# Kernel optimization log

Hardware: AMD Instinct MI355X
Metric: run time of the kernel (lower is better)

Reference implementation:

```python
import jax, jax.numpy as jnp
import numpy as np

V, E, H, L = 10000, 512, 512, 3   # vocab, embed dim, hidden, num decoder layers
SOS, EOS = 1, 2


def setup_inputs() -> dict:
    key = jax.random.key(0)
    ks = jax.random.split(key, 16)
    N, To, Ti = 32, 64, 512
    s = 0.05
    inp = {
        'padded_input': jax.random.randint(ks[0], (N, To), 0, V),
        'encoder_padded_outputs': jax.random.normal(ks[1], (N, Ti, H), jnp.float32),
        'emb': jax.random.normal(ks[2], (V, E), jnp.float32) * s,
        # layer 0 LSTMCell: input = embed + encoder context (E + H)
        'W_ih0': jax.random.normal(ks[3], (4 * H, E + H), jnp.float32) * s,
        'W_hh0': jax.random.normal(ks[4], (4 * H, H), jnp.float32) * s,
        'b_ih0': jnp.zeros((4 * H,), jnp.float32),
        'b_hh0': jnp.zeros((4 * H,), jnp.float32),
        # layers 1..L-1 LSTMCells (stacked)
        'W_ih_r': jax.random.normal(ks[5], (L - 1, 4 * H, H), jnp.float32) * s,
        'W_hh_r': jax.random.normal(ks[6], (L - 1, 4 * H, H), jnp.float32) * s,
        'b_ih_r': jnp.zeros((L - 1, 4 * H), jnp.float32),
        'b_hh_r': jnp.zeros((L - 1, 4 * H), jnp.float32),
        # MLP: Linear(2H -> H), Tanh, Linear(H -> V)
        'W1': jax.random.normal(ks[7], (H, 2 * H), jnp.float32) * s,
        'b1': jnp.zeros((H,), jnp.float32),
        'W2': jax.random.normal(ks[8], (V, H), jnp.float32) * s,
        'b2': jnp.zeros((V,), jnp.float32),
    }
    return inp


def _lstm_cell(x, h, c, Wi, Wh, bi, bh):
    # torch.nn.LSTMCell gate order: i, f, g, o
    g = x @ Wi.T + h @ Wh.T + bi + bh
    i, f, gg, o = jnp.split(g, 4, axis=-1)
    c2 = jax.nn.sigmoid(f) * c + jax.nn.sigmoid(i) * jnp.tanh(gg)
    h2 = jax.nn.sigmoid(o) * jnp.tanh(c2)
    return h2, c2


def reference(padded_input, encoder_padded_outputs, emb,
              W_ih0, W_hh0, b_ih0, b_hh0,
              W_ih_r, W_hh_r, b_ih_r, b_hh_r,
              W1, b1, W2, b2):
    N, To = padded_input.shape
    sos = jnp.full((N, 1), SOS, padded_input.dtype)
    eos = jnp.full((N, 1), EOS, padded_input.dtype)
    ys_in = jnp.concatenate([sos, padded_input], axis=1)    # [N, T]
    ys_out = jnp.concatenate([padded_input, eos], axis=1)   # [N, T]
    xs = jnp.transpose(emb[ys_in], (1, 0, 2))               # [T, N, E]

    def step(carry, x_t):
        h, c, att_c = carry                                  # h,c: [L,N,H]; att_c: [N,H]
        rnn_in = jnp.concatenate([x_t, att_c], axis=1)       # [N, E+H]
        h0, c0 = _lstm_cell(rnn_in, h[0], c[0], W_ih0, W_hh0, b_ih0, b_hh0)
        hs, cs = [h0], [c0]
        for l in range(L - 1):
            hl, cl = _lstm_cell(hs[-1], h[l + 1], c[l + 1],
                                W_ih_r[l], W_hh_r[l], b_ih_r[l], b_hh_r[l])
            hs.append(hl); cs.append(cl)
        r = hs[-1]                                           # [N, H]
        scores = jnp.einsum('nh,nth->nt', r, encoder_padded_outputs)
        w = jax.nn.softmax(scores, axis=-1)
        att = jnp.einsum('nt,nth->nh', w, encoder_padded_outputs)
        mlp_in = jnp.concatenate([r, att], axis=1)           # [N, 2H]
        y = jnp.tanh(mlp_in @ W1.T + b1) @ W2.T + b2         # [N, V]
        return (jnp.stack(hs), jnp.stack(cs), att), y

    h0 = jnp.zeros((L, N, H), encoder_padded_outputs.dtype)
    c0 = jnp.zeros((L, N, H), encoder_padded_outputs.dtype)
    a0 = jnp.zeros((N, H), encoder_padded_outputs.dtype)
    _, ys = jax.lax.scan(step, (h0, c0, a0), xs)             # [T, N, V]
    y_all = jnp.transpose(ys, (1, 0, 2))                     # [N, T, V]

    logp = jax.nn.log_softmax(y_all, axis=-1)
    nll = -jnp.take_along_axis(logp, ys_out[..., None], axis=-1)[..., 0]
    ce_loss = nll.mean()
    return y_all, ce_loss
```

## Files before the change

kernel.cpp:

```cpp
#include <hip/hip_runtime.h>
#include <hip/hip_bf16.h>
#include <hip/hip_fp16.h>

#define NB 32
#define TO 64
#define TT 65
#define TI 512
#define VV 10000
#define HH 512
#define G4 2048
#define SOS_ID 1
#define EOS_ID 2
#define NBLK 256

typedef unsigned uvec4 __attribute__((ext_vector_type(4)));
typedef unsigned uvec2 __attribute__((ext_vector_type(2)));
typedef _Float16 h2v __attribute__((ext_vector_type(2)));

__device__ __forceinline__ float cload1(const float* p) {
    unsigned v = __hip_atomic_load((const unsigned*)p,
                                   __ATOMIC_RELAXED, __HIP_MEMORY_SCOPE_AGENT);
    return __uint_as_float(v);
}
__device__ __forceinline__ float2 cload2(const float* p) {
    unsigned long long v = __hip_atomic_load((const unsigned long long*)p,
                                             __ATOMIC_RELAXED, __HIP_MEMORY_SCOPE_AGENT);
    float2 r;
    r.x = __uint_as_float((unsigned)(v & 0xffffffffull));
    r.y = __uint_as_float((unsigned)(v >> 32));
    return r;
}
__device__ __forceinline__ void cstore(float* p, float v) {
    __hip_atomic_store((unsigned*)p, __float_as_uint(v),
                       __ATOMIC_RELAXED, __HIP_MEMORY_SCOPE_AGENT);
}

__device__ __forceinline__ void gbar(int* flags, int g, int s, int& epoch) {
    asm volatile("s_waitcnt vmcnt(0) lgkmcnt(0)" ::: "memory");
    __syncthreads();
    epoch++;
    int tid = threadIdx.x;
    if (tid == 0)
        __hip_atomic_store(&flags[(g * 32 + s) * 16], epoch,
                           __ATOMIC_RELAXED, __HIP_MEMORY_SCOPE_AGENT);
    if (tid < 32) {
        for (;;) {
            int v = __hip_atomic_load(&flags[(g * 32 + tid) * 16],
                                      __ATOMIC_RELAXED, __HIP_MEMORY_SCOPE_AGENT);
            unsigned long long b = __ballot(v >= epoch);
            if ((b & 0xffffffffull) == 0xffffffffull) break;
            __builtin_amdgcn_s_sleep(1);
        }
    }
    __syncthreads();
}

__device__ __forceinline__ float bf2f(unsigned u16) {
    return __uint_as_float(u16 << 16);
}
__device__ __forceinline__ unsigned f2bf(float f) {
    unsigned u = __float_as_uint(f);
    return (u + 0x7fffu + ((u >> 16) & 1u)) >> 16;
}
__device__ __forceinline__ unsigned packh2(float a, float b) {
    __half2 h = __floats2half2_rn(a, b);
    return *(unsigned*)&h;
}
__device__ __forceinline__ h2v uash2(unsigned u) {
    union { unsigned u; h2v h; } c; c.u = u; return c.h;
}

template <int KQ4>
__device__ __forceinline__ void lstm_phase(
    const unsigned* __restrict__ Wtb, const float* __restrict__ bi,
    const float* __restrict__ bh, float* __restrict__ hout,
    float& creg, float* __restrict__ mlprow,
    float4* xs4, float* sg, float* sg2, int s, int n0,
    const float* __restrict__ pre) {
    int tid = threadIdx.x;
    int lane = tid & 63, wv = tid >> 6;
    const uvec2* wp = (const uvec2*)Wtb + (long)(wv * KQ4) * 2048 + (s * 64 + lane);
    const float4* xp = (const float4*)xs4 + wv * KQ4 * 4;
    float a0 = 0.f, a1 = 0.f, a2 = 0.f, a3 = 0.f;
#pragma unroll 4
    for (int kq = 0; kq < KQ4; kq++) {
        uvec2 u = wp[(long)kq * 2048];
        float w0 = bf2f(u.x & 0xffffu), w1 = bf2f(u.x >> 16);
        float w2 = bf2f(u.y & 0xffffu), w3 = bf2f(u.y >> 16);
        float4 x0 = xp[4 * kq], x1 = xp[4 * kq + 1];
        float4 x2 = xp[4 * kq + 2], x3 = xp[4 * kq + 3];
        a0 = fmaf(w0, x0.x, a0); a1 = fmaf(w0, x0.y, a1);
        a2 = fmaf(w0, x0.z, a2); a3 = fmaf(w0, x0.w, a3);
        a0 = fmaf(w1, x1.x, a0); a1 = fmaf(w1, x1.y, a1);
        a2 = fmaf(w1, x1.z, a2); a3 = fmaf(w1, x1.w, a3);
        a0 = fmaf(w2, x2.x, a0); a1 = fmaf(w2, x2.y, a1);
        a2 = fmaf(w2, x2.z, a2); a3 = fmaf(w2, x2.w, a3);
        a0 = fmaf(w3, x3.x, a0); a1 = fmaf(w3, x3.y, a1);
        a2 = fmaf(w3, x3.z, a2); a3 = fmaf(w3, x3.w, a3);
    }
    float4 r4; r4.x = a0; r4.y = a1; r4.z = a2; r4.w = a3;
    ((float4*)sg)[wv * 64 + lane] = r4;
    __syncthreads();
    {
        int c = tid >> 4, n = (tid >> 2) & 3, w4 = tid & 3;
        float sum = sg[((w4 * 4 + 0) * 64 + c) * 4 + n]
                  + sg[((w4 * 4 + 1) * 64 + c) * 4 + n]
                  + sg[((w4 * 4 + 2) * 64 + c) * 4 + n]
                  + sg[((w4 * 4 + 3) * 64 + c) * 4 + n];
        sg2[tid] = sum;
    }
    __syncthreads();
    if (tid < 64) {
        int gn = tid >> 4, gml = tid & 15, gm = s * 16 + gml;
        float ga[4];
#pragma unroll
        for (int q = 0; q < 4; q++) {
            int c = q * 16 + gml;
            const float* p = sg2 + c * 16 + gn * 4;
            ga[q] = p[0] + p[1] + p[2] + p[3];
        }
        float gi = ga[0] + bi[gm] + bh[gm];
        float gf = ga[1] + bi[512 + gm] + bh[512 + gm];
        float gg = ga[2] + bi[1024 + gm] + bh[1024 + gm];
        float go = ga[3] + bi[1536 + gm] + bh[1536 + gm];
        float si = 1.f / (1.f + expf(-gi));
        float sf = 1.f / (1.f + expf(-gf));
        float so = 1.f / (1.f + expf(-go));
        float c2 = sf * creg + si * tanhf(gg);
        creg = c2;
        float hv = so * tanhf(c2);
        cstore(&hout[(n0 + gn) * 512 + gm], hv);
        if (mlprow) mlprow[(long)(n0 + gn) * 1024 + gm] = hv;
    } else if (pre && tid >= 512 && tid < 768) {
        int k = 512 + (tid - 512) * 2;
        float2 va = cload2(pre + (n0 + 0) * 512 + (k - 512));
        float2 vb = cload2(pre + (n0 + 1) * 512 + (k - 512));
        float2 vc = cload2(pre + (n0 + 2) * 512 + (k - 512));
        float2 vd = cload2(pre + (n0 + 3) * 512 + (k - 512));
        float4 x0, x1;
        x0.x = va.x; x0.y = vb.x; x0.z = vc.x; x0.w = vd.x;
        x1.x = va.y; x1.y = vb.y; x1.z = vc.y; x1.w = vd.y;
        xs4[k] = x0; xs4[k + 1] = x1;
    }
}

__global__ __launch_bounds__(1024, 4) void decode_loop(
    const unsigned* __restrict__ Wtb0, const unsigned* __restrict__ Wtb1,
    const unsigned* __restrict__ Wtb2, const float* __restrict__ emb,
    const int* __restrict__ tokens, const float* __restrict__ enc,
    const float* __restrict__ b_ih0, const float* __restrict__ b_hh0,
    const float* __restrict__ b_ih_r, const float* __restrict__ b_hh_r,
    float* __restrict__ hbuf, float* __restrict__ pvec, float* __restrict__ pm,
    float* __restrict__ mlpin, int* flags) {
    __shared__ float4 xs4[1536];
    __shared__ float sg[4096];
    __shared__ float sg2[1024];
    __shared__ float wl[64];
    __shared__ unsigned short enct[32768];

    int tid = threadIdx.x, b = blockIdx.x;
    int g = b >> 5, s = b & 31;
    int epoch = 0;
    int n0 = g * 4;
    int na = n0 + (s >> 3), tiq = s & 7;
    float c0r = 0.f, c1r = 0.f, c2r = 0.f;

    {
        int tl = tid >> 4;
        int gb = (tid & 15) * 4;
        const float* ebase = enc + ((long)na * TI + tiq * 64 + tl) * HH;
#pragma unroll
        for (int q = 0; q < 4; q++) {
            int gg = gb + q;
            const float* ep = ebase + gg * 8;
            float4 lo = *(const float4*)ep;
            float4 hi = *(const float4*)(ep + 4);
            uvec4 pk;
            pk.x = f2bf(lo.x) | (f2bf(lo.y) << 16);
            pk.y = f2bf(lo.z) | (f2bf(lo.w) << 16);
            pk.z = f2bf(hi.x) | (f2bf(hi.y) << 16);
            pk.w = f2bf(hi.z) | (f2bf(hi.w) << 16);
            *(uvec4*)(enct + tl * 512 + (gg ^ (tl & 7)) * 8) = pk;
        }
    }
    __syncthreads();

    for (int t = 0; t < TT; t++) {
        int rp = t & 1;
        float* hOld = hbuf + rp * 3 * NB * HH;
        float* hNew = hbuf + (rp ^ 1) * 3 * NB * HH;
        float* h0r = hOld;
        float* h1r = hOld + NB * HH;
        float* h2r = hOld + 2 * NB * HH;
        float* h0w = hNew;
        float* h1w = hNew + NB * HH;
        float* h2w = hNew + 2 * NB * HH;

        if (t == 0) {
            if (tid < 768) {
                int k = tid * 2;
                float2 va, vb, vc, vd;
                if (k < 512) {
                    va = *(const float2*)(emb + (long)SOS_ID * 512 + k);
                    vb = va; vc = va; vd = va;
                } else if (k < 1024) {
                    va.x = va.y = 0.f; vb = va; vc = va; vd = va;
                } else {
                    int kk = k - 1024;
                    va = cload2(h0r + (n0 + 0) * 512 + kk);
                    vb = cload2(h0r + (n0 + 1) * 512 + kk);
                    vc = cload2(h0r + (n0 + 2) * 512 + kk);
                    vd = cload2(h0r + (n0 + 3) * 512 + kk);
                }
                float4 x0, x1;
                x0.x = va.x; x0.y = vb.x; x0.z = vc.x; x0.w = vd.x;
                x1.x = va.y; x1.y = vb.y; x1.z = vc.y; x1.w = vd.y;
                xs4[k] = x0; xs4[k + 1] = x1;
            }
            __syncthreads();
        } else {
            if (tid < 32) {
                int nn = tid >> 3, bb = tid & 7;
                sg[tid * 2] = cload1(&pm[((n0 + nn) * 8 + bb) * 2]);
                sg[tid * 2 + 1] = cload1(&pm[((n0 + nn) * 8 + bb) * 2 + 1]);
            }
            __syncthreads();
            {
                int nn = tid >> 8, hp = (tid & 255) * 2;
                float M = -1e30f;
#pragma unroll
                for (int bb = 0; bb < 8; bb++) M = fmaxf(M, sg[(nn * 8 + bb) * 2]);
                float al[8];
                float den = 0.f;
#pragma unroll
                for (int bb = 0; bb < 8; bb++) {
                    al[bb] = expf(sg[(nn * 8 + bb) * 2] - M);
                    den += al[bb] * sg[(nn * 8 + bb) * 2 + 1];
                }
                float inv = 1.f / den;
                float a0 = 0.f, a1 = 0.f;
#pragma unroll
                for (int bb = 0; bb < 8; bb++) {
                    float c = al[bb] * inv;
                    float2 v = cload2(&pvec[((long)(n0 + nn) * 8 + bb) * 512 + hp]);
                    a0 = fmaf(c, v.x, a0);
                    a1 = fmaf(c, v.y, a1);
                }
                sg[1024 + nn * 512 + hp] = a0;
                sg[1024 + nn * 512 + hp + 1] = a1;
            }
            __syncthreads();
            if (tid < 256) {
                int kk = tid * 2;
                float v0a = sg[1024 + 0 * 512 + kk], v0b = sg[1024 + 0 * 512 + kk + 1];
                float v1a = sg[1024 + 1 * 512 + kk], v1b = sg[1024 + 1 * 512 + kk + 1];
                float v2a = sg[1024 + 2 * 512 + kk], v2b = sg[1024 + 2 * 512 + kk + 1];
                float v3a = sg[1024 + 3 * 512 + kk], v3b = sg[1024 + 3 * 512 + kk + 1];
                if ((kk >> 4) == s) {
                    float* mp = mlpin + ((long)(t - 1) * NB + n0) * 1024 + 512 + kk;
                    mp[0] = v0a; mp[1] = v0b;
                    mp[1024] = v1a; mp[1025] = v1b;
                    mp[2048] = v2a; mp[2049] = v2b;
                    mp[3072] = v3a; mp[3073] = v3b;
                }
                float4 x0, x1;
                x0.x = v0a; x0.y = v1a; x0.z = v2a; x0.w = v3a;
                x1.x = v0b; x1.y = v1b; x1.z = v2b; x1.w = v3b;
                xs4[512 + kk] = x0; xs4[512 + kk + 1] = x1;
            }
            __syncthreads();
        }
        lstm_phase<24>(Wtb0, b_ih0, b_hh0, h0w, c0r, nullptr,
                       xs4, sg, sg2, s, n0, h1r);
        gbar(flags, g, s, epoch);

        if (tid < 256) {
            int k = tid * 2;
            float2 va = cload2(h0w + (n0 + 0) * 512 + k);
            float2 vb = cload2(h0w + (n0 + 1) * 512 + k);
            float2 vc = cload2(h0w + (n0 + 2) * 512 + k);
            float2 vd = cload2(h0w + (n0 + 3) * 512 + k);
            float4 x0, x1;
            x0.x = va.x; x0.y = vb.x; x0.z = vc.x; x0.w = vd.x;
            x1.x = va.y; x1.y = vb.y; x1.z = vc.y; x1.w = vd.y;
            xs4[k] = x0; xs4[k + 1] = x1;
        }
        __syncthreads();
        lstm_phase<16>(Wtb1, b_ih_r, b_hh_r, h1w, c1r, nullptr,
                       xs4, sg, sg2, s, n0, h2r);
        gbar(flags, g, s, epoch);

        if (tid < 256) {
            int k = tid * 2;
            float2 va = cload2(h1w + (n0 + 0) * 512 + k);
            float2 vb = cload2(h1w + (n0 + 1) * 512 + k);
            float2 vc = cload2(h1w + (n0 + 2) * 512 + k);
            float2 vd = cload2(h1w + (n0 + 3) * 512 + k);
            float4 x0, x1;
            x0.x = va.x; x0.y = vb.x; x0.z = vc.x; x0.w = vd.x;
            x1.x = va.y; x1.y = vb.y; x1.z = vc.y; x1.w = vd.y;
            xs4[k] = x0; xs4[k + 1] = x1;
        }
        __syncthreads();
        lstm_phase<16>(Wtb2, b_ih_r + G4, b_hh_r + G4, h2w, c2r,
                       mlpin + (long)t * NB * 1024,
                       xs4, sg, sg2, s, n0, nullptr);
        gbar(flags, g, s, epoch);

        if (tid < 512) sg2[tid] = cload1(h2w + na * 512 + tid);
        __syncthreads();
        {
            int tl = tid & 63, kh = tid >> 6;
            float acc = 0.f;
#pragma unroll
            for (int q = 0; q < 4; q++) {
                int gg = kh * 4 + q;
                uvec4 e = *(const uvec4*)(enct + tl * 512 + ((gg ^ (tl & 7)) * 8));
                const float* hp = sg2 + gg * 8;
                acc += bf2f(e.x & 0xffffu) * hp[0] + bf2f(e.x >> 16) * hp[1]
                     + bf2f(e.y & 0xffffu) * hp[2] + bf2f(e.y >> 16) * hp[3]
                     + bf2f(e.z & 0xffffu) * hp[4] + bf2f(e.z >> 16) * hp[5]
                     + bf2f(e.w & 0xffffu) * hp[6] + bf2f(e.w >> 16) * hp[7];
            }
            sg[tid] = acc;
        }
        __syncthreads();
        if (tid < 64) {
            float sv = 0.f;
#pragma unroll
            for (int w = 0; w < 16; w++) sv += sg[tid + 64 * w];
            float mb = sv;
#pragma unroll
            for (int o = 32; o > 0; o >>= 1) mb = fmaxf(mb, __shfl_xor(mb, o));
            float e = expf(sv - mb);
            float db = e;
#pragma unroll
            for (int o = 32; o > 0; o >>= 1) db += __shfl_xor(db, o);
            wl[tid] = e;
            if (tid == 0) {
                cstore(&pm[(na * 8 + tiq) * 2], mb);
                cstore(&pm[(na * 8 + tiq) * 2 + 1], db);
            }
        }
        __syncthreads();
        {
            int hp = (tid & 255) * 2, tis = (tid >> 8) * 16;
            int gb2 = hp >> 3, wrd = hp & 7;
            float a0 = 0.f, a1 = 0.f;
#pragma unroll 8
            for (int q = 0; q < 16; q++) {
                int tl = tis + q;
                unsigned u = *(const unsigned*)(enct + tl * 512 +
                                                ((gb2 ^ (tl & 7)) * 8) + wrd);
                float w = wl[tl];
                a0 = fmaf(w, bf2f(u & 0xffffu), a0);
                a1 = fmaf(w, bf2f(u >> 16), a1);
            }
            float* prt = sg + 1024;
            prt[(tid >> 8) * 512 + hp] = a0;
            prt[(tid >> 8) * 512 + hp + 1] = a1;
            __syncthreads();
            if (tid < 512) {
                int h = tid;
                float v = prt[h] + prt[512 + h] + prt[1024 + h] + prt[1536 + h];
                cstore(&pvec[((long)na * 8 + tiq) * 512 + h], v);
            }
            if (t + 1 < TT) {
                if (tid < 512) {
                    int k = tid;
                    int r0 = tokens[(n0 + 0) * TO + t];
                    int r1 = tokens[(n0 + 1) * TO + t];
                    int r2 = tokens[(n0 + 2) * TO + t];
                    int r3 = tokens[(n0 + 3) * TO + t];
                    float4 v;
                    v.x = emb[(long)r0 * 512 + k];
                    v.y = emb[(long)r1 * 512 + k];
                    v.z = emb[(long)r2 * 512 + k];
                    v.w = emb[(long)r3 * 512 + k];
                    xs4[k] = v;
                } else {
                    int k = tid - 512;
                    float4 v;
                    v.x = cload1(h0w + (n0 + 0) * 512 + k);
                    v.y = cload1(h0w + (n0 + 1) * 512 + k);
                    v.z = cload1(h0w + (n0 + 2) * 512 + k);
                    v.w = cload1(h0w + (n0 + 3) * 512 + k);
                    xs4[1024 + k] = v;
                }
            }
        }
        gbar(flags, g, s, epoch);
    }

    if (tid < 64) {
        int h = tiq * 64 + tid;
        float mm[8], dd[8], al[8];
        float M = -1e30f;
#pragma unroll
        for (int bb = 0; bb < 8; bb++) {
            mm[bb] = cload1(&pm[(na * 8 + bb) * 2]);
            dd[bb] = cload1(&pm[(na * 8 + bb) * 2 + 1]);
            M = fmaxf(M, mm[bb]);
        }
        float den = 0.f;
#pragma unroll
        for (int bb = 0; bb < 8; bb++) { al[bb] = expf(mm[bb] - M); den += al[bb] * dd[bb]; }
        float inv = 1.f / den;
        float v = 0.f;
#pragma unroll
        for (int bb = 0; bb < 8; bb++)
            v += (al[bb] * inv) * cload1(&pvec[((long)na * 8 + bb) * 512 + h]);
        mlpin[((long)(TT - 1) * NB + na) * 1024 + 512 + h] = v;
    }
}

__global__ void transpose_lstm_q(const float* __restrict__ Wih, int KA,
                                 const float* __restrict__ Whh,
                                 unsigned* __restrict__ Wtb) {
    int K = KA + 512;
    long total = (long)(K / 4) * 4096;
    for (long idx = (long)blockIdx.x * 256 + threadIdx.x; idx < total;
         idx += (long)gridDim.x * 256) {
        int c2 = (int)(idx % 4096);
        int kq = (int)(idx / 4096);
        int c = c2 >> 1, half = c2 & 1;
        int sI = c >> 6, r = c & 63, gg = r >> 4, ml = r & 15;
        int j = gg * 512 + sI * 16 + ml;
        int k0 = kq * 4 + half * 2, k1 = k0 + 1;
        float w0 = (k0 < KA) ? Wih[(long)j * KA + k0] : Whh[(long)j * 512 + (k0 - KA)];
        float w1 = (k1 < KA) ? Wih[(long)j * KA + k1] : Whh[(long)j * 512 + (k1 - KA)];
        Wtb[idx] = f2bf(w0) | (f2bf(w1) << 16);
    }
}

__global__ void transpose_w2_h2(const float* __restrict__ W2,
                                unsigned* __restrict__ Wh) {
    long total = (long)256 * 10240;
    for (long idx = (long)blockIdx.x * 256 + threadIdx.x; idx < total;
         idx += (long)gridDim.x * 256) {
        int j = (int)(idx % 10240);
        int kk = (int)(idx / 10240);
        float lo = 0.f, hi = 0.f;
        if (j < VV) {
            lo = W2[(long)j * 512 + 2 * kk];
            hi = W2[(long)j * 512 + 2 * kk + 1];
        }
        Wh[idx] = packh2(lo, hi);
    }
}

__global__ void transpose_cat(const float* __restrict__ A, int KA,
                              int J, int Jp, float* __restrict__ Wt) {
    long total = (long)KA * Jp;
    for (long idx = (long)blockIdx.x * 256 + threadIdx.x; idx < total;
         idx += (long)gridDim.x * 256) {
        int j = (int)(idx % Jp);
        int k = (int)(idx / Jp);
        Wt[idx] = (j < J) ? A[(long)j * KA + k] : 0.f;
    }
}

__global__ void gemm_mlp1(const float* __restrict__ Wt,
                          const float* __restrict__ X,
                          const float* __restrict__ bias,
                          unsigned* __restrict__ outh) {
    __shared__ float xs[64 * 12];
    int m0 = blockIdx.x * 8;
    int lane = threadIdx.x & 63;
    int wv = threadIdx.x >> 6;
    int jp = wv * 64 + lane;
    float acc0[8], acc1[8];
#pragma unroll
    for (int q = 0; q < 8; q++) { acc0[q] = 0.f; acc1[q] = 0.f; }
    for (int kc = 0; kc < 1024; kc += 64) {
        __syncthreads();
        for (int idx = threadIdx.x; idx < 512; idx += 256) {
            int k = idx >> 3, n = idx & 7;
            xs[k * 12 + n] = X[(long)(m0 + n) * 1024 + kc + k];
        }
        __syncthreads();
        const float2* wpp = (const float2*)(Wt + (long)kc * 512) + jp;
#pragma unroll 4
        for (int k = 0; k < 64; k++) {
            float2 w = wpp[(long)k * 256];
            const float4* xv = (const float4*)(xs + k * 12);
            float4 x0 = xv[0], x1 = xv[1];
            acc0[0] += w.x * x0.x; acc0[1] += w.x * x0.y;
            acc0[2] += w.x * x0.z; acc0[3] += w.x * x0.w;
            acc0[4] += w.x * x1.x; acc0[5] += w.x * x1.y;
            acc0[6] += w.x * x1.z; acc0[7] += w.x * x1.w;
            acc1[0] += w.y * x0.x; acc1[1] += w.y * x0.y;
            acc1[2] += w.y * x0.z; acc1[3] += w.y * x0.w;
            acc1[4] += w.y * x1.x; acc1[5] += w.y * x1.y;
            acc1[6] += w.y * x1.z; acc1[7] += w.y * x1.w;
        }
    }
    float b0 = bias[2 * jp], b1 = bias[2 * jp + 1];
#pragma unroll
    for (int n = 0; n < 8; n++) {
        float v0 = tanhf(acc0[n] + b0);
        float v1 = tanhf(acc1[n] + b1);
        outh[(long)(m0 + n) * 256 + jp] = packh2(v0, v1);
    }
}

__global__ void gemm_mlp2(const unsigned* __restrict__ Wh,
                          const unsigned* __restrict__ Xh,
                          const float* __restrict__ bias,
                          float* __restrict__ out) {
    __shared__ unsigned xs[256 * 36];
    int t = blockIdx.y;
    int m0 = t * 32;
    int lane = threadIdx.x & 63;
    int wv = threadIdx.x >> 6;
    int j0 = blockIdx.x * 256 + wv * 64 + lane;
    float acc0[32], acc1[32];
#pragma unroll
    for (int q = 0; q < 32; q++) { acc0[q] = 0.f; acc1[q] = 0.f; }
    for (int idx = threadIdx.x; idx < 8192; idx += 256) {
        int kk = idx & 255, n = idx >> 8;
        xs[kk * 36 + n] = Xh[(long)(m0 + n) * 256 + kk];
    }
    __syncthreads();
    const unsigned* wpp = Wh + j0;
#pragma unroll 2
    for (int kk = 0; kk < 256; kk++) {
        unsigned u0 = wpp[(long)kk * 10240];
        unsigned u1 = wpp[(long)kk * 10240 + 5120];
        h2v w0 = uash2(u0), w1 = uash2(u1);
        const uvec4* xv = (const uvec4*)(xs + kk * 36);
#pragma unroll
        for (int q = 0; q < 8; q++) {
            uvec4 x4 = xv[q];
            acc0[4 * q + 0] = __builtin_amdgcn_fdot2(uash2(x4.x), w0, acc0[4 * q + 0], false);
            acc0[4 * q + 1] = __builtin_amdgcn_fdot2(uash2(x4.y), w0, acc0[4 * q + 1], false);
            acc0[4 * q + 2] = __builtin_amdgcn_fdot2(uash2(x4.z), w0, acc0[4 * q + 2], false);
            acc0[4 * q + 3] = __builtin_amdgcn_fdot2(uash2(x4.w), w0, acc0[4 * q + 3], false);
            acc1[4 * q + 0] = __builtin_amdgcn_fdot2(uash2(x4.x), w1, acc1[4 * q + 0], false);
            acc1[4 * q + 1] = __builtin_amdgcn_fdot2(uash2(x4.y), w1, acc1[4 * q + 1], false);
            acc1[4 * q + 2] = __builtin_amdgcn_fdot2(uash2(x4.z), w1, acc1[4 * q + 2], false);
            acc1[4 * q + 3] = __builtin_amdgcn_fdot2(uash2(x4.w), w1, acc1[4 * q + 3], false);
        }
    }
#pragma unroll
    for (int nn = 0; nn < 32; nn++) {
        long row = (long)nn * TT + t;
        float* po = out + row * VV;
        int ja = j0, jb = j0 + 5120;
        po[ja] = acc0[nn] + bias[ja];
        if (jb < VV) po[jb] = acc1[nn] + bias[jb];
    }
}

__global__ void loss_rows(const float* __restrict__ out, const int* __restrict__ tokens,
                          float* __restrict__ nll) {
    __shared__ float red[256];
    int row = blockIdx.x;
    int n = row / TT, t = row % TT;
    const float* y = out + (long)row * VV;
    int tid = threadIdx.x;
    float m = -1e30f;
    for (int v = tid; v < VV; v += 256) m = fmaxf(m, y[v]);
    red[tid] = m;
    __syncthreads();
    for (int s = 128; s > 0; s >>= 1) {
        if (tid < s) red[tid] = fmaxf(red[tid], red[tid + s]);
        __syncthreads();
    }
    m = red[0];
    __syncthreads();
    float sum = 0.f;
    for (int v = tid; v < VV; v += 256) sum += expf(y[v] - m);
    red[tid] = sum;
    __syncthreads();
    for (int s = 128; s > 0; s >>= 1) {
        if (tid < s) red[tid] += red[tid + s];
        __syncthreads();
    }
    if (tid == 0) {
        int target = (t < TO) ? tokens[n * TO + t] : EOS_ID;
        nll[row] = m + logf(red[0]) - y[target];
    }
}

__global__ void loss_final(const float* __restrict__ nll, float* __restrict__ out_loss) {
    __shared__ float red[256];
    int tid = threadIdx.x;
    float s = 0.f;
    for (int i = tid; i < NB * TT; i += 256) s += nll[i];
    red[tid] = s;
    __syncthreads();
    for (int k = 128; k > 0; k >>= 1) {
        if (tid < k) red[tid] += red[tid + k];
        __syncthreads();
    }
    if (tid == 0) *out_loss = red[0] / (float)(NB * TT);
}

extern "C" void kernel_launch(void* const* d_in, const int* in_sizes, int n_in,
                              void* d_out, int out_size, void* d_ws, size_t ws_size,
                              hipStream_t stream) {
    const int* padded   = (const int*)d_in[0];
    const float* enc    = (const float*)d_in[1];
    const float* emb    = (const float*)d_in[2];
    const float* W_ih0  = (const float*)d_in[3];
    const float* W_hh0  = (const float*)d_in[4];
    const float* b_ih0  = (const float*)d_in[5];
    const float* b_hh0  = (const float*)d_in[6];
    const float* W_ih_r = (const float*)d_in[7];
    const float* W_hh_r = (const float*)d_in[8];
    const float* b_ih_r = (const float*)d_in[9];
    const float* b_hh_r = (const float*)d_in[10];
    const float* W1     = (const float*)d_in[11];
    const float* b1     = (const float*)d_in[12];
    const float* W2     = (const float*)d_in[13];
    const float* b2     = (const float*)d_in[14];
    float* out = (float*)d_out;
    float* ws  = (float*)d_ws;

    unsigned* Wtb0 = (unsigned*)ws;
    unsigned* Wtb1 = Wtb0 + 384 * 4096;
    unsigned* Wtb2 = Wtb1 + 256 * 4096;
    unsigned* Wh   = Wtb2 + 256 * 4096;
    float* Wm1  = (float*)(Wh + 256 * 10240);
    float* hbuf = Wm1 + 1024 * 512;
    float* mlpin= hbuf + 2 * 3 * NB * HH;
    unsigned* y1h = (unsigned*)(mlpin + (long)TT * NB * 1024);
    float* pvec = (float*)(y1h + (long)TT * NB * 256);
    float* pm   = pvec + 32 * 8 * 512;
    float* nll  = pm + 512;
    int*   flags= (int*)(nll + 2080);

    hipMemsetAsync(hbuf, 0, (size_t)(2 * 3 * NB * HH) * sizeof(float), stream);
    hipMemsetAsync(flags, 0, 8 * 32 * 16 * sizeof(int), stream);

    transpose_cat<<<1024, 256, 0, stream>>>(W1, 1024, 512, 512, Wm1);
    transpose_lstm_q<<<2048, 256, 0, stream>>>(W_ih0, 1024, W_hh0, Wtb0);
    transpose_lstm_q<<<2048, 256, 0, stream>>>(W_ih_r, 512, W_hh_r, Wtb1);
    transpose_lstm_q<<<2048, 256, 0, stream>>>(W_ih_r + 2048 * 512, 512,
                                               W_hh_r + 2048 * 512, Wtb2);
    transpose_w2_h2<<<2048, 256, 0, stream>>>(W2, Wh);

    decode_loop<<<NBLK, 1024, 0, stream>>>(Wtb0, Wtb1, Wtb2, emb, padded, enc,
                                           b_ih0, b_hh0, b_ih_r, b_hh_r,
                                           hbuf, pvec, pm, mlpin, flags);

    gemm_mlp1<<<260, 256, 0, stream>>>(Wm1, mlpin, b1, y1h);
    gemm_mlp2<<<dim3(20, TT), 256, 0, stream>>>(Wh, y1h, b2, out);
    loss_rows<<<NB * TT, 256, 0, stream>>>(out, padded, nll);
    loss_final<<<1, 256, 0, stream>>>(nll, out + (long)NB * TT * VV);
}
```

Measured before the change: 2.218 ms.

## Replace fp16 dot2 vocab projection GEMM with bf16 MFMA kernel

```diff
diff --git a/kernel.cpp b/kernel.cpp
--- a/kernel.cpp
+++ b/kernel.cpp
@@ -15,7 +15,9 @@
 
 typedef unsigned uvec4 __attribute__((ext_vector_type(4)));
 typedef unsigned uvec2 __attribute__((ext_vector_type(2)));
-typedef _Float16 h2v __attribute__((ext_vector_type(2)));
+typedef short bf16x4 __attribute__((ext_vector_type(4)));
+typedef short bf16x8 __attribute__((ext_vector_type(8)));
+typedef float f32x4 __attribute__((ext_vector_type(4)));
 
 __device__ __forceinline__ float cload1(const float* p) {
     unsigned v = __hip_atomic_load((const unsigned*)p,
@@ -62,12 +64,8 @@
     unsigned u = __float_as_uint(f);
     return (u + 0x7fffu + ((u >> 16) & 1u)) >> 16;
 }
-__device__ __forceinline__ unsigned packh2(float a, float b) {
-    __half2 h = __floats2half2_rn(a, b);
-    return *(unsigned*)&h;
-}
-__device__ __forceinline__ h2v uash2(unsigned u) {
-    union { unsigned u; h2v h; } c; c.u = u; return c.h;
+__device__ __forceinline__ unsigned packbf2(float a, float b) {
+    return f2bf(a) | (f2bf(b) << 16);
 }
 
 template <int KQ4>
@@ -433,19 +431,19 @@
     }
 }
 
-__global__ void transpose_w2_h2(const float* __restrict__ W2,
-                                unsigned* __restrict__ Wh) {
-    long total = (long)256 * 10240;
+__global__ void transpose_w2_bf(const float* __restrict__ W2,
+                                unsigned* __restrict__ Wb) {
+    long total = (long)10240 * 256;
     for (long idx = (long)blockIdx.x * 256 + threadIdx.x; idx < total;
          idx += (long)gridDim.x * 256) {
-        int j = (int)(idx % 10240);
-        int kk = (int)(idx / 10240);
+        int kk = (int)(idx & 255);
+        int j = (int)(idx >> 8);
         float lo = 0.f, hi = 0.f;
         if (j < VV) {
             lo = W2[(long)j * 512 + 2 * kk];
             hi = W2[(long)j * 512 + 2 * kk + 1];
         }
-        Wh[idx] = packh2(lo, hi);
+        Wb[idx] = packbf2(lo, hi);
     }
 }
 
@@ -463,7 +461,7 @@
 __global__ void gemm_mlp1(const float* __restrict__ Wt,
                           const float* __restrict__ X,
                           const float* __restrict__ bias,
-                          unsigned* __restrict__ outh) {
+                          unsigned* __restrict__ outb) {
     __shared__ float xs[64 * 12];
     int m0 = blockIdx.x * 8;
     int lane = threadIdx.x & 63;
@@ -500,56 +498,65 @@
     for (int n = 0; n < 8; n++) {
         float v0 = tanhf(acc0[n] + b0);
         float v1 = tanhf(acc1[n] + b1);
-        outh[(long)(m0 + n) * 256 + jp] = packh2(v0, v1);
-    }
-}
-
-__global__ void gemm_mlp2(const unsigned* __restrict__ Wh,
-                          const unsigned* __restrict__ Xh,
-                          const float* __restrict__ bias,
-                          float* __restrict__ out) {
-    __shared__ unsigned xs[256 * 36];
+        outb[(long)(m0 + n) * 256 + jp] = packbf2(v0, v1);
+    }
+}
+
+__device__ __forceinline__ bf16x8 ldfrag(const unsigned short* p) {
+    bf16x4 lo = *(const bf16x4*)p;
+    bf16x4 hi = *(const bf16x4*)(p + 16);
+    bf16x8 r;
+    r[0] = lo[0]; r[1] = lo[1]; r[2] = lo[2]; r[3] = lo[3];
+    r[4] = hi[0]; r[5] = hi[1]; r[6] = hi[2]; r[7] = hi[3];
+    return r;
+}
+
+__global__ __launch_bounds__(256) void gemm_mlp2_mfma(
+    const unsigned short* __restrict__ Wb2,
+    const unsigned short* __restrict__ Yb,
+    const float* __restrict__ bias,
+    float* __restrict__ out) {
     int t = blockIdx.y;
     int m0 = t * 32;
-    int lane = threadIdx.x & 63;
-    int wv = threadIdx.x >> 6;
-    int j0 = blockIdx.x * 256 + wv * 64 + lane;
-    float acc0[32], acc1[32];
-#pragma unroll
-    for (int q = 0; q < 32; q++) { acc0[q] = 0.f; acc1[q] = 0.f; }
-    for (int idx = threadIdx.x; idx < 8192; idx += 256) {
-        int kk = idx & 255, n = idx >> 8;
-        xs[kk * 36 + n] = Xh[(long)(m0 + n) * 256 + kk];
-    }
-    __syncthreads();
-    const unsigned* wpp = Wh + j0;
+    int l = threadIdx.x & 63, w = threadIdx.x >> 6;
+    int colbase = blockIdx.x * 256 + w * 64;
+    int r16 = l & 15, kq = l >> 4;
+    f32x4 acc[2][4];
+#pragma unroll
+    for (int i = 0; i < 2; i++)
+#pragma unroll
+        for (int j = 0; j < 4; j++) acc[i][j] = (f32x4){0.f, 0.f, 0.f, 0.f};
+
+    const unsigned short* a0p = Yb + (long)(m0 + r16) * 512 + kq * 4;
+    const unsigned short* a1p = a0p + 16 * 512;
 #pragma unroll 2
-    for (int kk = 0; kk < 256; kk++) {
-        unsigned u0 = wpp[(long)kk * 10240];
-        unsigned u1 = wpp[(long)kk * 10240 + 5120];
-        h2v w0 = uash2(u0), w1 = uash2(u1);
-        const uvec4* xv = (const uvec4*)(xs + kk * 36);
-#pragma unroll
-        for (int q = 0; q < 8; q++) {
-            uvec4 x4 = xv[q];
-            acc0[4 * q + 0] = __builtin_amdgcn_fdot2(uash2(x4.x), w0, acc0[4 * q + 0], false);
-            acc0[4 * q + 1] = __builtin_amdgcn_fdot2(uash2(x4.y), w0, acc0[4 * q + 1], false);
-            acc0[4 * q + 2] = __builtin_amdgcn_fdot2(uash2(x4.z), w0, acc0[4 * q + 2], false);
-            acc0[4 * q + 3] = __builtin_amdgcn_fdot2(uash2(x4.w), w0, acc0[4 * q + 3], false);
-            acc1[4 * q + 0] = __builtin_amdgcn_fdot2(uash2(x4.x), w1, acc1[4 * q + 0], false);
-            acc1[4 * q + 1] = __builtin_amdgcn_fdot2(uash2(x4.y), w1, acc1[4 * q + 1], false);
-            acc1[4 * q + 2] = __builtin_amdgcn_fdot2(uash2(x4.z), w1, acc1[4 * q + 2], false);
-            acc1[4 * q + 3] = __builtin_amdgcn_fdot2(uash2(x4.w), w1, acc1[4 * q + 3], false);
-        }
-    }
-#pragma unroll
-    for (int nn = 0; nn < 32; nn++) {
-        long row = (long)nn * TT + t;
-        float* po = out + row * VV;
-        int ja = j0, jb = j0 + 5120;
-        po[ja] = acc0[nn] + bias[ja];
-        if (jb < VV) po[jb] = acc1[nn] + bias[jb];
-    }
+    for (int ks = 0; ks < 16; ks++) {
+        int kb = ks * 32;
+        bf16x8 a0 = ldfrag(a0p + kb);
+        bf16x8 a1 = ldfrag(a1p + kb);
+#pragma unroll
+        for (int ct = 0; ct < 4; ct++) {
+            const unsigned short* bp =
+                Wb2 + (long)(colbase + ct * 16 + r16) * 512 + kb + kq * 4;
+            bf16x8 bf = ldfrag(bp);
+            acc[0][ct] = __builtin_amdgcn_mfma_f32_16x16x32_bf16(a0, bf, acc[0][ct], 0, 0, 0);
+            acc[1][ct] = __builtin_amdgcn_mfma_f32_16x16x32_bf16(a1, bf, acc[1][ct], 0, 0, 0);
+        }
+    }
+#pragma unroll
+    for (int mi = 0; mi < 2; mi++)
+#pragma unroll
+        for (int ct = 0; ct < 4; ct++) {
+            int col = colbase + ct * 16 + r16;
+            if (col < VV) {
+                float bv = bias[col];
+#pragma unroll
+                for (int r = 0; r < 4; r++) {
+                    int nn = mi * 16 + kq * 4 + r;
+                    out[((long)nn * TT + t) * VV + col] = acc[mi][ct][r] + bv;
+                }
+            }
+        }
 }
 
 __global__ void loss_rows(const float* __restrict__ out, const int* __restrict__ tokens,
@@ -621,12 +628,12 @@
     unsigned* Wtb0 = (unsigned*)ws;
     unsigned* Wtb1 = Wtb0 + 384 * 4096;
     unsigned* Wtb2 = Wtb1 + 256 * 4096;
-    unsigned* Wh   = Wtb2 + 256 * 4096;
-    float* Wm1  = (float*)(Wh + 256 * 10240);
+    unsigned* Wb2u = Wtb2 + 256 * 4096;
+    float* Wm1  = (float*)(Wb2u + 10240 * 256);
     float* hbuf = Wm1 + 1024 * 512;
     float* mlpin= hbuf + 2 * 3 * NB * HH;
-    unsigned* y1h = (unsigned*)(mlpin + (long)TT * NB * 1024);
-    float* pvec = (float*)(y1h + (long)TT * NB * 256);
+    unsigned* y1b = (unsigned*)(mlpin + (long)TT * NB * 1024);
+    float* pvec = (float*)(y1b + (long)TT * NB * 256);
     float* pm   = pvec + 32 * 8 * 512;
     float* nll  = pm + 512;
     int*   flags= (int*)(nll + 2080);
@@ -639,14 +646,15 @@
     transpose_lstm_q<<<2048, 256, 0, stream>>>(W_ih_r, 512, W_hh_r, Wtb1);
     transpose_lstm_q<<<2048, 256, 0, stream>>>(W_ih_r + 2048 * 512, 512,
                                                W_hh_r + 2048 * 512, Wtb2);
-    transpose_w2_h2<<<2048, 256, 0, stream>>>(W2, Wh);
+    transpose_w2_bf<<<2048, 256, 0, stream>>>(W2, Wb2u);
 
     decode_loop<<<NBLK, 1024, 0, stream>>>(Wtb0, Wtb1, Wtb2, emb, padded, enc,
                                            b_ih0, b_hh0, b_ih_r, b_hh_r,
                                            hbuf, pvec, pm, mlpin, flags);
 
-    gemm_mlp1<<<260, 256, 0, stream>>>(Wm1, mlpin, b1, y1h);
-    gemm_mlp2<<<dim3(20, TT), 256, 0, stream>>>(Wh, y1h, b2, out);
+    gemm_mlp1<<<260, 256, 0, stream>>>(Wm1, mlpin, b1, y1b);
+    gemm_mlp2_mfma<<<dim3(40, TT), 256, 0, stream>>>(
+        (const unsigned short*)Wb2u, (const unsigned short*)y1b, b2, out);
     loss_rows<<<NB * TT, 256, 0, stream>>>(out, padded, nll);
     loss_final<<<1, 256, 0, stream>>>(nll, out + (long)NB * TT * VV);
 }
```

Measured after the change: 2.204 ms, median of 2. About the same (-0.7%).
